# Kernel optimization log

Hardware: AMD Instinct MI355X
Metric: run time of the kernel (lower is better)

## Reference

```python
import jax, jax.numpy as jnp
import numpy as np

NUM_ITERS = 3


def squash(s):
    # s: [..., V]
    sq = (s ** 2).sum(-1, keepdims=True)
    return sq * s / ((1.0 + sq) * jnp.sqrt(sq))


def setup_inputs() -> dict:
    key = jax.random.key(0)
    kx, kw = jax.random.split(key)
    B, O, I, V, D = 32, 1, 4096, 512, 8
    x = jax.random.normal(kx, (B, I, D), dtype=jnp.float32)
    W = 0.01 * jax.random.normal(kw, (O, I, V, D), dtype=jnp.float32)
    return {"x": x, "W": W}


def reference(x, W):
    B = x.shape[0]
    O, I, V, _ = W.shape
    # x_hat[b,o,i,v] = sum_d W[o,i,v,d] * x[b,i,d]
    x_hat = jnp.einsum('oivd,bid->boiv', W, x)  # [B,O,I,V]
    x_hat_d = jax.lax.stop_gradient(x_hat)

    b = jnp.zeros((B, O, I), dtype=x.dtype)
    for it in range(NUM_ITERS):
        c = jax.nn.softmax(b, axis=1)  # over out caps
        if it == NUM_ITERS - 1:
            outputs = squash((c[:, :, :, None] * x_hat).sum(-2, keepdims=True))
        else:
            outputs = squash((c[:, :, :, None] * x_hat_d).sum(-2, keepdims=True))
            b = b + (outputs * x_hat_d).sum(-1)

    outputs = outputs.squeeze(-2)  # [B,O,V]
    # decode_idx == -1 branch
    classes = jax.nn.softmax(jnp.sqrt((outputs ** 2).sum(2)), axis=1)  # [B,O]
    max_idx = jnp.argmax(classes, axis=1)  # [B]
    masked = jax.nn.one_hot(max_idx, O, dtype=outputs.dtype)  # [B,O]
    t = (outputs * masked[:, :, None]).sum(axis=1)[:, None, :]  # [B,1,V]
    return (t, outputs)
```

## Files before the change

kernel.cpp:

```cpp
#include <hip/hip_runtime.h>
#include <stdint.h>


#define NB 32
#define NI 4096
#define NV 512
#define ND 8
#define NK 32768
#define KB 128
#define KSB (NK / KB)
#define KSW (KSB / 4)
#define KSTEPS (KSW / 16)

typedef __fp16 f16x8 __attribute__((ext_vector_type(8)));
typedef __fp16 f16x2 __attribute__((ext_vector_type(2)));
typedef float  f32x16 __attribute__((ext_vector_type(16)));

__global__ __launch_bounds__(256) void x_prep(
    const float* __restrict__ x, __fp16* __restrict__ xh,
    __fp16* __restrict__ xl)
{
    const int tid = blockIdx.x * 256 + threadIdx.x;
    const int b = tid & 31;
    const int g = tid >> 5;

    const float4* xp = (const float4*)(x + (size_t)b * NK + (size_t)g * 8);
    const float4 f0 = xp[0];
    const float4 f1 = xp[1];

    const f16x2 h0 = __builtin_amdgcn_cvt_pkrtz(f0.x, f0.y);
    const f16x2 h1 = __builtin_amdgcn_cvt_pkrtz(f0.z, f0.w);
    const f16x2 h2 = __builtin_amdgcn_cvt_pkrtz(f1.x, f1.y);
    const f16x2 h3 = __builtin_amdgcn_cvt_pkrtz(f1.z, f1.w);
    const f16x2 l0 = __builtin_amdgcn_cvt_pkrtz(f0.x - (float)h0.x, f0.y - (float)h0.y);
    const f16x2 l1 = __builtin_amdgcn_cvt_pkrtz(f0.z - (float)h1.x, f0.w - (float)h1.y);
    const f16x2 l2 = __builtin_amdgcn_cvt_pkrtz(f1.x - (float)h2.x, f1.y - (float)h2.y);
    const f16x2 l3 = __builtin_amdgcn_cvt_pkrtz(f1.z - (float)h3.x, f1.w - (float)h3.y);

    const f16x8 h = {h0.x, h0.y, h1.x, h1.y, h2.x, h2.y, h3.x, h3.y};
    const f16x8 l = {l0.x, l0.y, l1.x, l1.y, l2.x, l2.y, l3.x, l3.y};
    ((f16x8*)xh)[tid] = h;
    ((f16x8*)xl)[tid] = l;
}

__global__ __launch_bounds__(256) void caps_mfma(
    const float* __restrict__ W, const __fp16* __restrict__ xh,
    const __fp16* __restrict__ xl, float* __restrict__ partial)
{
    const int t    = threadIdx.x;
    const int lane = t & 63;
    const int wave = t >> 6;
    const int half = lane >> 5;
    const int ln32 = lane & 31;

    const int kb = blockIdx.x & (KB - 1);
    const int vg = blockIdx.x >> 7;
    const int v0 = vg * 32;
    const int k0 = kb * KSB + wave * KSW;
    const int g0 = (k0 >> 3) + half;

    f32x16 acc;
#pragma unroll
    for (int r = 0; r < 16; ++r) acc[r] = 0.0f;

    const __fp16* ah = xh + ((size_t)g0 * 32 + ln32) * 8;
    const __fp16* al = xl + ((size_t)g0 * 32 + ln32) * 8;
    const float4* wp = (const float4*)(W + ((size_t)g0 * NV + v0 + ln32) * ND);

#pragma unroll 2
    for (int s = 0; s < KSTEPS; ++s) {
        const float4 w0 = wp[0];
        const float4 w1 = wp[1];
        wp += 2 * NV * ND / 4;
        const f16x8 a_hi = *(const f16x8*)ah;  ah += 2 * 32 * 8;
        const f16x8 a_lo = *(const f16x8*)al;  al += 2 * 32 * 8;

        const f16x2 h01 = __builtin_amdgcn_cvt_pkrtz(w0.x, w0.y);
        const f16x2 h23 = __builtin_amdgcn_cvt_pkrtz(w0.z, w0.w);
        const f16x2 h45 = __builtin_amdgcn_cvt_pkrtz(w1.x, w1.y);
        const f16x2 h67 = __builtin_amdgcn_cvt_pkrtz(w1.z, w1.w);
        const f16x8 b = {h01.x, h01.y, h23.x, h23.y, h45.x, h45.y, h67.x, h67.y};

        acc = __builtin_amdgcn_mfma_f32_32x32x16_f16(a_hi, b, acc, 0, 0, 0);
        acc = __builtin_amdgcn_mfma_f32_32x32x16_f16(a_lo, b, acc, 0, 0, 0);
    }

    __shared__ float red[4 * 1024];
#pragma unroll
    for (int r = 0; r < 16; ++r)
        red[wave * 1024 + r * 64 + lane] = acc[r];
    __syncthreads();

#pragma unroll
    for (int j = 0; j < 4; ++j) {
        const int s  = t + j * 256;
        const float val = red[s] + red[1024 + s] + red[2048 + s] + red[3072 + s];
        const int r   = s >> 6;
        const int ln  = s & 63;
        const int row = (r & 3) + 8 * (r >> 2) + 4 * (ln >> 5);
        const int col = ln & 31;
        partial[((size_t)kb * NB + row) * NV + v0 + col] = val;
    }
}

__global__ __launch_bounds__(512) void caps_finish(
    const float* __restrict__ partial, float* __restrict__ out)
{
    const int v = threadIdx.x;
    const int b = blockIdx.x;

    float s = 0.0f;
#pragma unroll 16
    for (int g = 0; g < KB; ++g)
        s += partial[((size_t)g * NB + b) * NV + v];

    float sq = s * s;
#pragma unroll
    for (int off = 32; off > 0; off >>= 1)
        sq += __shfl_xor(sq, off, 64);

    __shared__ float red[8];
    if ((v & 63) == 0) red[v >> 6] = sq;
    __syncthreads();
    float tot = 0.0f;
#pragma unroll
    for (int wv = 0; wv < 8; ++wv) tot += red[wv];

    const float factor = sqrtf(tot) / (1.0f + tot);
    const float r = s * factor;

    out[(size_t)b * NV + v]           = r;
    out[NB * NV + (size_t)b * NV + v] = r;
}

extern "C" void kernel_launch(void* const* d_in, const int* in_sizes, int n_in,
                              void* d_out, int out_size, void* d_ws, size_t ws_size,
                              hipStream_t stream) {
    const float* x = (const float*)d_in[0];
    const float* W = (const float*)d_in[1];
    float* out     = (float*)d_out;

    __fp16* xh     = (__fp16*)d_ws;
    __fp16* xl     = xh + (size_t)NB * NK;
    float*  partial = (float*)(xl + (size_t)NB * NK);

    x_prep<<<(NB * NK / 8) / 256, 256, 0, stream>>>(x, xh, xl);
    caps_mfma<<<KB * 16, 256, 0, stream>>>(W, xh, xl, partial);
    caps_finish<<<NB, 512, 0, stream>>>(partial, out);
}
```

Before: 110.1 us.

## Store split-K partials in fp16 and add a parallel two-stage reduction

The MFMA kernel now writes its per-K-block partial sums as fp16, which halves the partial buffer traffic. A new intermediate kernel with 512 blocks reduces groups of 8 partials into fp32, so the final kernel sums only 16 partials instead of 128 across just 32 blocks. The aim is to cut the serial, low-occupancy tail reduction. In exchange it adds one extra kernel launch and rounds each partial to fp16, which loses precision.

```diff
diff --git a/kernel.cpp b/kernel.cpp
--- a/kernel.cpp
+++ b/kernel.cpp
@@ -11,6 +11,7 @@
 #define KSB (NK / KB)
 #define KSW (KSB / 4)
 #define KSTEPS (KSW / 16)
+#define NG (KB / 8)
 
 typedef __fp16 f16x8 __attribute__((ext_vector_type(8)));
 typedef __fp16 f16x2 __attribute__((ext_vector_type(2)));
@@ -45,7 +46,7 @@
 
 __global__ __launch_bounds__(256) void caps_mfma(
     const float* __restrict__ W, const __fp16* __restrict__ xh,
-    const __fp16* __restrict__ xl, float* __restrict__ partial)
+    const __fp16* __restrict__ xl, __fp16* __restrict__ partial_h)
 {
     const int t    = threadIdx.x;
     const int lane = t & 63;
@@ -99,20 +100,40 @@
         const int ln  = s & 63;
         const int row = (r & 3) + 8 * (r >> 2) + 4 * (ln >> 5);
         const int col = ln & 31;
-        partial[((size_t)kb * NB + row) * NV + v0 + col] = val;
+        partial_h[((size_t)kb * NB + row) * NV + v0 + col] = (__fp16)val;
     }
 }
 
+__global__ __launch_bounds__(256) void caps_reduce8(
+    const __fp16* __restrict__ partial_h, float* __restrict__ partial2)
+{
+    const int t = threadIdx.x;
+    const int b = blockIdx.x & 31;
+    const int g = blockIdx.x >> 5;
+
+    const __fp16* p = partial_h + ((size_t)(g * 8) * NB + b) * NV + 2 * t;
+    float s0 = 0.0f, s1 = 0.0f;
+#pragma unroll
+    for (int j = 0; j < 8; ++j) {
+        const f16x2 h = *(const f16x2*)(p + (size_t)j * NB * NV);
+        s0 += (float)h.x;
+        s1 += (float)h.y;
+    }
+
+    float2 o = {s0, s1};
+    ((float2*)(partial2 + ((size_t)g * NB + b) * NV))[t] = o;
+}
+
 __global__ __launch_bounds__(512) void caps_finish(
-    const float* __restrict__ partial, float* __restrict__ out)
+    const float* __restrict__ partial2, float* __restrict__ out)
 {
     const int v = threadIdx.x;
     const int b = blockIdx.x;
 
     float s = 0.0f;
-#pragma unroll 16
-    for (int g = 0; g < KB; ++g)
-        s += partial[((size_t)g * NB + b) * NV + v];
+#pragma unroll
+    for (int g = 0; g < NG; ++g)
+        s += partial2[((size_t)g * NB + b) * NV + v];
 
     float sq = s * s;
 #pragma unroll
@@ -140,11 +161,13 @@
     const float* W = (const float*)d_in[1];
     float* out     = (float*)d_out;
 
-    __fp16* xh     = (__fp16*)d_ws;
-    __fp16* xl     = xh + (size_t)NB * NK;
-    float*  partial = (float*)(xl + (size_t)NB * NK);
+    __fp16* xh       = (__fp16*)d_ws;
+    __fp16* xl       = xh + (size_t)NB * NK;
+    __fp16* partialh = xl + (size_t)NB * NK;
+    float*  partial2 = (float*)(partialh + (size_t)KB * NB * NV);
 
     x_prep<<<(NB * NK / 8) / 256, 256, 0, stream>>>(x, xh, xl);
-    caps_mfma<<<KB * 16, 256, 0, stream>>>(W, xh, xl, partial);
-    caps_finish<<<NB, 512, 0, stream>>>(partial, out);
+    caps_mfma<<<KB * 16, 256, 0, stream>>>(W, xh, xl, partialh);
+    caps_reduce8<<<NG * NB, 256, 0, stream>>>(partialh, partial2);
+    caps_finish<<<NB, 512, 0, stream>>>(partial2, out);
 }
```

Result: no change. 108.2 us (-1.8%).
